# Kernel tuning notes

Hardware: AMD Instinct MI355X
Metric: run time of the kernel (lower is better)

Reference implementation:

```python
import jax, jax.numpy as jnp
import numpy as np

NIPSIN = [0, 1, 2]
MAXNIPSIN = max(NIPSIN)
MAXNUMTYPE = 4
NWAVE = 8
CUTOFF = 5.0
NUMATOM = 20000
NEDGE = 500000
HIDDEN = 128

_index_para = np.concatenate([np.full(3 ** i, j, dtype=np.int64) for j, i in enumerate(NIPSIN)])
P_ORI = int(_index_para.shape[0])  # 13 for nipsin=[0,1,2]
IPSIN = len(NIPSIN)
ONEHOT = jnp.asarray(np.eye(IPSIN, dtype=np.float32)[_index_para])  # [P_ORI, IPSIN]
INDEX_PARA = jnp.asarray(_index_para)
DFEAT = IPSIN * NWAVE


def _angular(dist_vec):
    # faithful to GetDensity.angular: concat of tensor-product powers of dist_vec
    n = dist_vec.shape[0]
    parts = [jnp.ones((n, 1), dist_vec.dtype), dist_vec]
    orbital = dist_vec
    num = 2
    for ip in range(1, MAXNIPSIN):
        orbital = jnp.einsum('ij,ik->ijk', orbital, dist_vec).reshape(n, -1)
        if ip + 1 == NIPSIN[num]:
            parts.append(orbital)
            num += 1
    return jnp.concatenate(parts, axis=1)  # [n, P_ORI]


def setup_inputs() -> dict:
    key = jax.random.key(0)
    ks = jax.random.split(key, 12)
    cart = jax.random.normal(ks[0], (NUMATOM, 3), dtype=jnp.float32) * 4.0
    neigh_list = jax.random.randint(ks[1], (2, NEDGE), 0, NUMATOM)
    shifts = jnp.zeros((NEDGE, 3), dtype=jnp.float32)
    species = jax.random.randint(ks[2], (NUMATOM,), 0, MAXNUMTYPE)
    rs = jax.random.uniform(ks[3], (MAXNUMTYPE, NWAVE), dtype=jnp.float32) * CUTOFF
    inta = jax.random.uniform(ks[4], (MAXNUMTYPE, NWAVE), dtype=jnp.float32) * 1.5 + 0.2
    params = 2.0 * jax.random.normal(ks[5], (MAXNUMTYPE, NWAVE), dtype=jnp.float32) - 1.0
    s1 = 1.0 / np.sqrt(DFEAT)
    s2 = 1.0 / np.sqrt(HIDDEN)
    return {
        'cart': cart, 'neigh_list': neigh_list, 'shifts': shifts, 'species': species,
        'rs': rs, 'inta': inta, 'params': params,
        'w1_0': jax.random.normal(ks[6], (DFEAT, HIDDEN), dtype=jnp.float32) * s1,
        'b1_0': jnp.zeros((HIDDEN,), dtype=jnp.float32),
        'w2_0': jax.random.normal(ks[7], (HIDDEN, DFEAT), dtype=jnp.float32) * s2,
        'b2_0': jnp.zeros((DFEAT,), dtype=jnp.float32),
        'w1_1': jax.random.normal(ks[8], (DFEAT, HIDDEN), dtype=jnp.float32) * s1,
        'b1_1': jnp.zeros((HIDDEN,), dtype=jnp.float32),
        'w2_1': jax.random.normal(ks[9], (HIDDEN, DFEAT), dtype=jnp.float32) * s2,
        'b2_1': jnp.zeros((DFEAT,), dtype=jnp.float32),
    }


def reference(cart, neigh_list, shifts, species, rs, inta, params,
              w1_0, b1_0, w2_0, b2_0, w1_1, b1_1, w2_1, b2_1):
    center = neigh_list[0]
    neigh = neigh_list[1]
    dist_vec = cart[center] - cart[neigh] - shifts            # [E,3]
    distances = jnp.linalg.norm(dist_vec, axis=-1)            # [E]
    fc = jnp.square(0.5 * jnp.cos(distances * (np.pi / CUTOFF)) + 0.5)
    ns = species[neigh]                                       # [E]
    # vectorized per-type gaussian (same math as the masked type loop)
    gauss = jnp.exp(-inta[ns] * jnp.square(distances[:, None] - rs[ns])) * params[ns]  # [E,NWAVE]
    ang = _angular(dist_vec)                                  # [E,P_ORI]
    radial = ang[:, :, None] * fc[:, None, None] * gauss[:, None, :]  # [E,P_ORI,NWAVE]
    orbital = jax.ops.segment_sum(radial, center, num_segments=NUMATOM)  # [A,P_ORI,NWAVE]
    density = jnp.einsum('apw,pi->aiw', jnp.square(orbital), ONEHOT).reshape(NUMATOM, -1)
    for (w1, b1, w2, b2) in ((w1_0, b1_0, w2_0, b2_0), (w1_1, b1_1, w2_1, b2_1)):
        output = jnp.tanh(density @ w1 + b1) @ w2 + b2        # [A,IPSIN*NWAVE]
        expand = output[neigh].reshape(-1, IPSIN, NWAVE)[:, INDEX_PARA, :]  # [E,P_ORI,NWAVE]
        sum_w = jax.ops.segment_sum(expand * radial, center, num_segments=NUMATOM)
        density = jnp.einsum('apw,pi->aiw', jnp.square(sum_w), ONEHOT).reshape(NUMATOM, -1)
    return density
```

## Files before the change

kernel.cpp:

```cpp
#include <hip/hip_runtime.h>
#include <math.h>

#define NATOM_FEAT 24
#define PORI 13
#define NW 8
#define CAP 64
#define CH 32
#define ANG_S 13
#define OG_S 26
#define WSLICE (CH * (ANG_S + OG_S))
#define HID 128

#define WAVE_SYNC() do { asm volatile("s_waitcnt lgkmcnt(0)" ::: "memory"); \
                         __builtin_amdgcn_wave_barrier(); } while (0)

__global__ void zero_k(int* __restrict__ p, int n)
{
    int i = blockIdx.x * blockDim.x + threadIdx.x;
    if (i < n) p[i] = 0;
}

__global__ void fill_k(const int* __restrict__ nl,
                       int* __restrict__ cursor,
                       const float* __restrict__ cart,
                       const float* __restrict__ shifts,
                       const int* __restrict__ species,
                       const float* __restrict__ g_rs,
                       const float* __restrict__ g_inta,
                       const float* __restrict__ g_par,
                       float4* __restrict__ slots,
                       int E)
{
    __shared__ float s_rs[32], s_in[32], s_pa[32];
    if (threadIdx.x < 32) {
        s_rs[threadIdx.x] = g_rs[threadIdx.x];
        s_in[threadIdx.x] = g_inta[threadIdx.x];
        s_pa[threadIdx.x] = g_par[threadIdx.x];
    }
    __syncthreads();
    int e = blockIdx.x * blockDim.x + threadIdx.x;
    if (e >= E) return;
    int c = nl[e];
    int n = nl[E + e];
    float dx = cart[3*c+0] - cart[3*n+0] - shifts[3*e+0];
    float dy = cart[3*c+1] - cart[3*n+1] - shifts[3*e+1];
    float dz = cart[3*c+2] - cart[3*n+2] - shifts[3*e+2];
    float r  = sqrtf(dx*dx + dy*dy + dz*dz);
    float fcb = 0.5f * cosf(r * 0.6283185307179586f) + 0.5f;
    float fc  = fcb * fcb;
    int sb = species[n] * NW;
    float g[NW];
    #pragma unroll
    for (int w = 0; w < NW; ++w) {
        float dr = r - s_rs[sb + w];
        g[w] = __expf(-s_in[sb + w] * dr * dr) * s_pa[sb + w] * fc;
    }
    int ofs = atomicAdd(&cursor[c], 1);
    if (ofs < CAP) {
        size_t si = ((size_t)c * CAP + ofs) * 4;
        slots[si + 0] = make_float4(dx, dy, dz, __int_as_float(n));
        slots[si + 1] = make_float4(g[0], g[1], g[2], g[3]);
        slots[si + 2] = make_float4(g[4], g[5], g[6], g[7]);
    }
}

template<bool HASOUT, bool MLP>
__global__ __launch_bounds__(256, 8)
void atom_pass(const float4* __restrict__ slots,
               const int* __restrict__ cursor,
               const float* __restrict__ outp_in,
               const float* __restrict__ w1, const float* __restrict__ b1,
               const float* __restrict__ w2, const float* __restrict__ b2,
               float* __restrict__ out,
               int A)
{
    __shared__ __align__(16) float smem[4 * WSLICE];
    int lane = threadIdx.x & 63;
    int wid  = threadIdx.x >> 6;
    float* ls = smem + wid * WSLICE;
    float* ls_ang = ls;
    float* ls_og  = ls + CH * ANG_S;
    float* orb_s = ls;
    float* dvec  = ls + 104;
    float* tvec  = ls + 128;

    int a = blockIdx.x * 4 + wid;
    if (a >= A) return;
    int cnt = min(cursor[a], CAP);

    int p  = lane >> 2, wq = lane & 3;
    int ip = (p == 0) ? 0 : ((p < 4) ? 1 : 2);
    int ogb = ip * NW + 2 * wq;

    float acc0 = 0.0f, acc1 = 0.0f;

    for (int s = 0; s < cnt; s += CH) {
        int m = min(CH, cnt - s);
        if (lane < m) {
            size_t si = ((size_t)a * CAP + s + lane) * 4;
            float4 D = slots[si + 0];
            float4 G = slots[si + 1];
            float4 H = slots[si + 2];
            float go[NW] = { G.x, G.y, G.z, G.w, H.x, H.y, H.z, H.w };
            float ax = D.x, ay = D.y, az = D.z;

            float* ar = ls_ang + lane * ANG_S;
            ar[0]  = 1.0f;
            ar[1]  = ax;    ar[2]  = ay;    ar[3]  = az;
            ar[4]  = ax*ax; ar[5]  = ax*ay; ar[6]  = ax*az;
            ar[7]  = ay*ax; ar[8]  = ay*ay; ar[9]  = ay*az;
            ar[10] = az*ax; ar[11] = az*ay; ar[12] = az*az;

            float2* ogr = (float2*)(ls_og + lane * OG_S);
            if (HASOUT) {
                const float4* orow = (const float4*)(outp_in + (size_t)__float_as_int(D.w) * NATOM_FEAT);
                float4 o0 = orow[0], o1 = orow[1], o2 = orow[2];
                float4 o3 = orow[3], o4 = orow[4], o5 = orow[5];
                const float* oa = (const float*)&o0;
                const float* ob = (const float*)&o1;
                const float* oc = (const float*)&o2;
                const float* od = (const float*)&o3;
                const float* oe = (const float*)&o4;
                const float* of = (const float*)&o5;
                #pragma unroll
                for (int q = 0; q < 4; ++q) {
                    ogr[q]     = make_float2(go[q]*oa[q], go[q+4]*ob[q]);
                    ogr[4 + q] = make_float2(go[q]*oc[q], go[q+4]*od[q]);
                    ogr[8 + q] = make_float2(go[q]*oe[q], go[q+4]*of[q]);
                }
            } else {
                #pragma unroll
                for (int q = 0; q < 4; ++q) {
                    float2 v = make_float2(go[q], go[q+4]);
                    ogr[q] = v; ogr[4 + q] = v; ogr[8 + q] = v;
                }
            }
        }
        WAVE_SYNC();
        if (lane < 52) {
            for (int j = 0; j < m; ++j) {
                float  av = ls_ang[j * ANG_S + p];
                float2 ov = *(const float2*)(ls_og + j * OG_S + ogb);
                acc0 += av * ov.x;
                acc1 += av * ov.y;
            }
        }
        WAVE_SYNC();
    }

    if (lane < 52) {
        orb_s[p * NW + wq]     = acc0 * acc0;
        orb_s[p * NW + wq + 4] = acc1 * acc1;
    }
    WAVE_SYNC();

    if (lane < NATOM_FEAT) {
        int i = lane >> 3, ww = lane & 7;
        float sum;
        if (i == 0) {
            sum = orb_s[ww];
        } else if (i == 1) {
            sum = orb_s[NW + ww] + orb_s[2*NW + ww] + orb_s[3*NW + ww];
        } else {
            sum = 0.0f;
            #pragma unroll
            for (int q = 4; q < PORI; ++q) sum += orb_s[q*NW + ww];
        }
        if (MLP) dvec[lane] = sum;
        else     out[(size_t)a * NATOM_FEAT + lane] = sum;
    }

    if (MLP) {
        WAVE_SYNC();
        float h0 = b1[lane], h1 = b1[lane + 64];
        #pragma unroll
        for (int j = 0; j < NATOM_FEAT; ++j) {
            float d = dvec[j];
            h0 += d * w1[j * HID + lane];
            h1 += d * w1[j * HID + lane + 64];
        }
        float e0 = __expf(2.0f * h0), e1 = __expf(2.0f * h1);
        tvec[lane]      = 1.0f - 2.0f / (e0 + 1.0f);
        tvec[lane + 64] = 1.0f - 2.0f / (e1 + 1.0f);
        WAVE_SYNC();
        int j  = (lane < 24) ? lane : lane - 24;
        int hb = (lane < 24) ? 0 : 64;
        float part = 0.0f;
        if (lane < 48) {
            #pragma unroll 8
            for (int h = 0; h < 64; ++h)
                part += tvec[hb + h] * w2[(hb + h) * NATOM_FEAT + j];
        }
        float other = __shfl(part, lane + 24);
        if (lane < NATOM_FEAT)
            out[(size_t)a * NATOM_FEAT + lane] = b2[lane] + part + other;
    }
}

extern "C" void kernel_launch(void* const* d_in, const int* in_sizes, int n_in,
                              void* d_out, int out_size, void* d_ws, size_t ws_size,
                              hipStream_t stream)
{
    const float* cart    = (const float*)d_in[0];
    const int*   nl      = (const int*)d_in[1];
    const float* shifts  = (const float*)d_in[2];
    const int*   species = (const int*)d_in[3];
    const float* rs      = (const float*)d_in[4];
    const float* inta    = (const float*)d_in[5];
    const float* params  = (const float*)d_in[6];
    const float* w1_0 = (const float*)d_in[7];
    const float* b1_0 = (const float*)d_in[8];
    const float* w2_0 = (const float*)d_in[9];
    const float* b2_0 = (const float*)d_in[10];
    const float* w1_1 = (const float*)d_in[11];
    const float* b1_1 = (const float*)d_in[12];
    const float* w2_1 = (const float*)d_in[13];
    const float* b2_1 = (const float*)d_in[14];

    const int A = in_sizes[0] / 3;
    const int E = in_sizes[1] / 2;

    char* ws = (char*)d_ws;
    float4* slots = (float4*)ws;              ws += (size_t)A * CAP * 64;
    int*   cursor = (int*)ws;                 ws += (size_t)A * 4;
    float* outpA  = (float*)ws;               ws += (size_t)A * NATOM_FEAT * 4;
    float* outpB  = (float*)ws;               ws += (size_t)A * NATOM_FEAT * 4;
    float* dout   = (float*)d_out;

    const int BLK = 256;
    const int gridE = (E + BLK - 1) / BLK;
    const int gridA = (A + BLK - 1) / BLK;
    const int gridP = (A + 3) / 4;

    zero_k<<<gridA, BLK, 0, stream>>>(cursor, A);
    fill_k<<<gridE, BLK, 0, stream>>>(nl, cursor, cart, shifts, species,
                                      rs, inta, params, slots, E);

    atom_pass<false, true><<<gridP, 256, 0, stream>>>(slots, cursor,
                                                      nullptr, w1_0, b1_0, w2_0, b2_0, outpA, A);
    atom_pass<true, true><<<gridP, 256, 0, stream>>>(slots, cursor,
                                                     outpA, w1_1, b1_1, w2_1, b2_1, outpB, A);
    atom_pass<true, false><<<gridP, 256, 0, stream>>>(slots, cursor,
                                                      outpB, nullptr, nullptr, nullptr, nullptr, dout, A);
}
```

Before: 113.3 us.

## Store only displacement and packed neighbor/species per slot; recompute gaussians per pass

```diff
diff --git a/kernel.cpp b/kernel.cpp
--- a/kernel.cpp
+++ b/kernel.cpp
@@ -25,19 +25,9 @@
                        const float* __restrict__ cart,
                        const float* __restrict__ shifts,
                        const int* __restrict__ species,
-                       const float* __restrict__ g_rs,
-                       const float* __restrict__ g_inta,
-                       const float* __restrict__ g_par,
                        float4* __restrict__ slots,
                        int E)
 {
-    __shared__ float s_rs[32], s_in[32], s_pa[32];
-    if (threadIdx.x < 32) {
-        s_rs[threadIdx.x] = g_rs[threadIdx.x];
-        s_in[threadIdx.x] = g_inta[threadIdx.x];
-        s_pa[threadIdx.x] = g_par[threadIdx.x];
-    }
-    __syncthreads();
     int e = blockIdx.x * blockDim.x + threadIdx.x;
     if (e >= E) return;
     int c = nl[e];
@@ -45,29 +35,19 @@
     float dx = cart[3*c+0] - cart[3*n+0] - shifts[3*e+0];
     float dy = cart[3*c+1] - cart[3*n+1] - shifts[3*e+1];
     float dz = cart[3*c+2] - cart[3*n+2] - shifts[3*e+2];
-    float r  = sqrtf(dx*dx + dy*dy + dz*dz);
-    float fcb = 0.5f * cosf(r * 0.6283185307179586f) + 0.5f;
-    float fc  = fcb * fcb;
-    int sb = species[n] * NW;
-    float g[NW];
-    #pragma unroll
-    for (int w = 0; w < NW; ++w) {
-        float dr = r - s_rs[sb + w];
-        g[w] = __expf(-s_in[sb + w] * dr * dr) * s_pa[sb + w] * fc;
-    }
+    int packed = n | (species[n] << 20);
     int ofs = atomicAdd(&cursor[c], 1);
-    if (ofs < CAP) {
-        size_t si = ((size_t)c * CAP + ofs) * 4;
-        slots[si + 0] = make_float4(dx, dy, dz, __int_as_float(n));
-        slots[si + 1] = make_float4(g[0], g[1], g[2], g[3]);
-        slots[si + 2] = make_float4(g[4], g[5], g[6], g[7]);
-    }
+    if (ofs < CAP)
+        slots[(size_t)c * CAP + ofs] = make_float4(dx, dy, dz, __int_as_float(packed));
 }
 
 template<bool HASOUT, bool MLP>
 __global__ __launch_bounds__(256, 8)
 void atom_pass(const float4* __restrict__ slots,
                const int* __restrict__ cursor,
+               const float* __restrict__ g_rs,
+               const float* __restrict__ g_inta,
+               const float* __restrict__ g_par,
                const float* __restrict__ outp_in,
                const float* __restrict__ w1, const float* __restrict__ b1,
                const float* __restrict__ w2, const float* __restrict__ b2,
@@ -97,12 +77,40 @@
     for (int s = 0; s < cnt; s += CH) {
         int m = min(CH, cnt - s);
         if (lane < m) {
-            size_t si = ((size_t)a * CAP + s + lane) * 4;
-            float4 D = slots[si + 0];
-            float4 G = slots[si + 1];
-            float4 H = slots[si + 2];
-            float go[NW] = { G.x, G.y, G.z, G.w, H.x, H.y, H.z, H.w };
+            float4 D = slots[(size_t)a * CAP + s + lane];
             float ax = D.x, ay = D.y, az = D.z;
+            int packed = __float_as_int(D.w);
+            int n  = packed & 0xFFFFF;
+            int sp = packed >> 20;
+
+            float r  = sqrtf(ax*ax + ay*ay + az*az);
+            float fcb = 0.5f * __cosf(r * 0.6283185307179586f) + 0.5f;
+            float fc  = fcb * fcb;
+            const float4* rs4 = (const float4*)(g_rs   + sp * NW);
+            const float4* in4 = (const float4*)(g_inta + sp * NW);
+            const float4* pa4 = (const float4*)(g_par  + sp * NW);
+            float4 r0 = rs4[0], r1 = rs4[1];
+            float4 i0 = in4[0], i1 = in4[1];
+            float4 p0 = pa4[0], p1 = pa4[1];
+            float go[NW];
+            {
+                const float* rr = (const float*)&r0;
+                const float* ii = (const float*)&i0;
+                const float* pp = (const float*)&p0;
+                #pragma unroll
+                for (int w = 0; w < 4; ++w) {
+                    float dr = r - rr[w];
+                    go[w] = __expf(-ii[w] * dr * dr) * pp[w] * fc;
+                }
+                const float* rr1 = (const float*)&r1;
+                const float* ii1 = (const float*)&i1;
+                const float* pp1 = (const float*)&p1;
+                #pragma unroll
+                for (int w = 0; w < 4; ++w) {
+                    float dr = r - rr1[w];
+                    go[w + 4] = __expf(-ii1[w] * dr * dr) * pp1[w] * fc;
+                }
+            }
 
             float* ar = ls_ang + lane * ANG_S;
             ar[0]  = 1.0f;
@@ -113,7 +121,7 @@
 
             float2* ogr = (float2*)(ls_og + lane * OG_S);
             if (HASOUT) {
-                const float4* orow = (const float4*)(outp_in + (size_t)__float_as_int(D.w) * NATOM_FEAT);
+                const float4* orow = (const float4*)(outp_in + (size_t)n * NATOM_FEAT);
                 float4 o0 = orow[0], o1 = orow[1], o2 = orow[2];
                 float4 o3 = orow[3], o4 = orow[4], o5 = orow[5];
                 const float* oa = (const float*)&o0;
@@ -221,7 +229,7 @@
     const int E = in_sizes[1] / 2;
 
     char* ws = (char*)d_ws;
-    float4* slots = (float4*)ws;              ws += (size_t)A * CAP * 64;
+    float4* slots = (float4*)ws;              ws += (size_t)A * CAP * 16;
     int*   cursor = (int*)ws;                 ws += (size_t)A * 4;
     float* outpA  = (float*)ws;               ws += (size_t)A * NATOM_FEAT * 4;
     float* outpB  = (float*)ws;               ws += (size_t)A * NATOM_FEAT * 4;
@@ -233,13 +241,12 @@
     const int gridP = (A + 3) / 4;
 
     zero_k<<<gridA, BLK, 0, stream>>>(cursor, A);
-    fill_k<<<gridE, BLK, 0, stream>>>(nl, cursor, cart, shifts, species,
-                                      rs, inta, params, slots, E);
-
-    atom_pass<false, true><<<gridP, 256, 0, stream>>>(slots, cursor,
+    fill_k<<<gridE, BLK, 0, stream>>>(nl, cursor, cart, shifts, species, slots, E);
+
+    atom_pass<false, true><<<gridP, 256, 0, stream>>>(slots, cursor, rs, inta, params,
                                                       nullptr, w1_0, b1_0, w2_0, b2_0, outpA, A);
-    atom_pass<true, true><<<gridP, 256, 0, stream>>>(slots, cursor,
+    atom_pass<true, true><<<gridP, 256, 0, stream>>>(slots, cursor, rs, inta, params,
                                                      outpA, w1_1, b1_1, w2_1, b2_1, outpB, A);
-    atom_pass<true, false><<<gridP, 256, 0, stream>>>(slots, cursor,
+    atom_pass<true, false><<<gridP, 256, 0, stream>>>(slots, cursor, rs, inta, params,
                                                       outpB, nullptr, nullptr, nullptr, nullptr, dout, A);
 }
```

New measurement: 120.9 us. 6.7% more time.

## Two-pass bucketed binning of edges before per-atom slot fill

Applied to the files above, without the earlier changes.

```diff
diff --git a/kernel.cpp b/kernel.cpp
--- a/kernel.cpp
+++ b/kernel.cpp
@@ -11,6 +11,12 @@
 #define WSLICE (CH * (ANG_S + OG_S))
 #define HID 128
 
+#define APB 32
+#define NBKT 626
+#define BCAP 1024
+#define P1T 512
+#define P1E 8
+
 #define WAVE_SYNC() do { asm volatile("s_waitcnt lgkmcnt(0)" ::: "memory"); \
                          __builtin_amdgcn_wave_barrier(); } while (0)
 
@@ -20,48 +26,117 @@
     if (i < n) p[i] = 0;
 }
 
-__global__ void fill_k(const int* __restrict__ nl,
-                       int* __restrict__ cursor,
-                       const float* __restrict__ cart,
-                       const float* __restrict__ shifts,
-                       const int* __restrict__ species,
-                       const float* __restrict__ g_rs,
-                       const float* __restrict__ g_inta,
-                       const float* __restrict__ g_par,
-                       float4* __restrict__ slots,
-                       int E)
+__global__ void cart4_k(const float* __restrict__ cart, const int* __restrict__ species,
+                        float4* __restrict__ cart4, int A)
+{
+    int i = blockIdx.x * blockDim.x + threadIdx.x;
+    if (i < A)
+        cart4[i] = make_float4(cart[3*i], cart[3*i+1], cart[3*i+2],
+                               __int_as_float(species[i]));
+}
+
+__global__ __launch_bounds__(P1T)
+void bin_k(const int* __restrict__ nl,
+           const float4* __restrict__ cart4,
+           const float* __restrict__ shifts,
+           int* __restrict__ bcur,
+           float4* __restrict__ bin,
+           int E)
+{
+    __shared__ int histo[NBKT];
+    __shared__ int base[NBKT];
+    int tid = threadIdx.x;
+    for (int i = tid; i < NBKT; i += P1T) histo[i] = 0;
+    __syncthreads();
+
+    int e0 = blockIdx.x * (P1T * P1E);
+    int bk[P1E], ofs[P1E];
+    float4 rec[P1E];
+    #pragma unroll
+    for (int k = 0; k < P1E; ++k) {
+        int e = e0 + k * P1T + tid;
+        bk[k] = -1;
+        if (e < E) {
+            int c = nl[e];
+            int n = nl[E + e];
+            float4 cc = cart4[c];
+            float4 cn = cart4[n];
+            float dx = cc.x - cn.x - shifts[3*e+0];
+            float dy = cc.y - cn.y - shifts[3*e+1];
+            float dz = cc.z - cn.z - shifts[3*e+2];
+            int sp = __float_as_int(cn.w);
+            int bits = n | (sp << 20) | ((c & (APB-1)) << 22);
+            rec[k] = make_float4(dx, dy, dz, __int_as_float(bits));
+            bk[k]  = c >> 5;
+            ofs[k] = atomicAdd(&histo[bk[k]], 1);
+        }
+    }
+    __syncthreads();
+    for (int i = tid; i < NBKT; i += P1T)
+        base[i] = histo[i] ? atomicAdd(&bcur[i * 16], histo[i]) : 0;
+    __syncthreads();
+    #pragma unroll
+    for (int k = 0; k < P1E; ++k) {
+        if (bk[k] >= 0) {
+            int idx = base[bk[k]] + ofs[k];
+            if (idx < BCAP) bin[(size_t)bk[k] * BCAP + idx] = rec[k];
+        }
+    }
+}
+
+__global__ __launch_bounds__(256)
+void slot_k(const float4* __restrict__ bin,
+            const int* __restrict__ bcur,
+            const float* __restrict__ g_rs,
+            const float* __restrict__ g_inta,
+            const float* __restrict__ g_par,
+            float4* __restrict__ slots,
+            int* __restrict__ cursor,
+            int A)
 {
     __shared__ float s_rs[32], s_in[32], s_pa[32];
-    if (threadIdx.x < 32) {
-        s_rs[threadIdx.x] = g_rs[threadIdx.x];
-        s_in[threadIdx.x] = g_inta[threadIdx.x];
-        s_pa[threadIdx.x] = g_par[threadIdx.x];
-    }
-    __syncthreads();
-    int e = blockIdx.x * blockDim.x + threadIdx.x;
-    if (e >= E) return;
-    int c = nl[e];
-    int n = nl[E + e];
-    float dx = cart[3*c+0] - cart[3*n+0] - shifts[3*e+0];
-    float dy = cart[3*c+1] - cart[3*n+1] - shifts[3*e+1];
-    float dz = cart[3*c+2] - cart[3*n+2] - shifts[3*e+2];
-    float r  = sqrtf(dx*dx + dy*dy + dz*dz);
-    float fcb = 0.5f * cosf(r * 0.6283185307179586f) + 0.5f;
-    float fc  = fcb * fcb;
-    int sb = species[n] * NW;
-    float g[NW];
-    #pragma unroll
-    for (int w = 0; w < NW; ++w) {
-        float dr = r - s_rs[sb + w];
-        g[w] = __expf(-s_in[sb + w] * dr * dr) * s_pa[sb + w] * fc;
-    }
-    int ofs = atomicAdd(&cursor[c], 1);
-    if (ofs < CAP) {
-        size_t si = ((size_t)c * CAP + ofs) * 4;
-        slots[si + 0] = make_float4(dx, dy, dz, __int_as_float(n));
-        slots[si + 1] = make_float4(g[0], g[1], g[2], g[3]);
-        slots[si + 2] = make_float4(g[4], g[5], g[6], g[7]);
-    }
+    __shared__ int lcnt[APB];
+    int tid = threadIdx.x;
+    if (tid < 32) {
+        s_rs[tid] = g_rs[tid];
+        s_in[tid] = g_inta[tid];
+        s_pa[tid] = g_par[tid];
+    }
+    if (tid >= 32 && tid < 32 + APB) lcnt[tid - 32] = 0;
+    __syncthreads();
+
+    int b  = blockIdx.x;
+    int c0 = b * APB;
+    int cnt = min(bcur[b * 16], BCAP);
+
+    for (int i = tid; i < cnt; i += 256) {
+        float4 rec = bin[(size_t)b * BCAP + i];
+        int bits = __float_as_int(rec.w);
+        int n    = bits & 0xFFFFF;
+        int sp   = (bits >> 20) & 3;
+        int clow = (bits >> 22) & (APB - 1);
+        int rank = atomicAdd(&lcnt[clow], 1);
+        if (rank < CAP) {
+            float dx = rec.x, dy = rec.y, dz = rec.z;
+            float r  = sqrtf(dx*dx + dy*dy + dz*dz);
+            float fcb = 0.5f * cosf(r * 0.6283185307179586f) + 0.5f;
+            float fc  = fcb * fcb;
+            int sb = sp * NW;
+            float g[NW];
+            #pragma unroll
+            for (int w = 0; w < NW; ++w) {
+                float dr = r - s_rs[sb + w];
+                g[w] = __expf(-s_in[sb + w] * dr * dr) * s_pa[sb + w] * fc;
+            }
+            size_t si = ((size_t)(c0 + clow) * CAP + rank) * 4;
+            slots[si + 0] = make_float4(dx, dy, dz, __int_as_float(n));
+            slots[si + 1] = make_float4(g[0], g[1], g[2], g[3]);
+            slots[si + 2] = make_float4(g[4], g[5], g[6], g[7]);
+        }
+    }
+    __syncthreads();
+    if (tid < APB && c0 + tid < A)
+        cursor[c0 + tid] = min(lcnt[tid], CAP);
 }
 
 template<bool HASOUT, bool MLP>
@@ -222,19 +297,23 @@
 
     char* ws = (char*)d_ws;
     float4* slots = (float4*)ws;              ws += (size_t)A * CAP * 64;
+    float4* bin   = (float4*)ws;              ws += (size_t)NBKT * BCAP * 16;
+    float4* cart4 = (float4*)ws;              ws += (size_t)A * 16;
+    int*   bcur   = (int*)ws;                 ws += (size_t)NBKT * 16 * 4;
     int*   cursor = (int*)ws;                 ws += (size_t)A * 4;
     float* outpA  = (float*)ws;               ws += (size_t)A * NATOM_FEAT * 4;
     float* outpB  = (float*)ws;               ws += (size_t)A * NATOM_FEAT * 4;
     float* dout   = (float*)d_out;
 
     const int BLK = 256;
-    const int gridE = (E + BLK - 1) / BLK;
     const int gridA = (A + BLK - 1) / BLK;
     const int gridP = (A + 3) / 4;
-
-    zero_k<<<gridA, BLK, 0, stream>>>(cursor, A);
-    fill_k<<<gridE, BLK, 0, stream>>>(nl, cursor, cart, shifts, species,
-                                      rs, inta, params, slots, E);
+    const int grid1 = (E + P1T * P1E - 1) / (P1T * P1E);
+
+    zero_k<<<(NBKT * 16 + BLK - 1) / BLK, BLK, 0, stream>>>(bcur, NBKT * 16);
+    cart4_k<<<gridA, BLK, 0, stream>>>(cart, species, cart4, A);
+    bin_k<<<grid1, P1T, 0, stream>>>(nl, cart4, shifts, bcur, bin, E);
+    slot_k<<<NBKT, 256, 0, stream>>>(bin, bcur, rs, inta, params, slots, cursor, A);
 
     atom_pass<false, true><<<gridP, 256, 0, stream>>>(slots, cursor,
                                                       nullptr, w1_0, b1_0, w2_0, b2_0, outpA, A);
```

New measurement: 116.3 us. +2.7%, slower.
